# Optimization experiments

Measured on AMD Instinct MI355X. Metric: run time of the kernel, lower is better.

Reference implementation:

```python
import jax, jax.numpy as jnp
import numpy as np

N_RAYS = 32768
N_SAMPLES = N_RAYS * 32  # 1,048,576
FDIM = 32
HID = 64
RGB_HID = 64
THRESHOLD = 1e-4  # early_termination_threshold


def setup_inputs() -> dict:
    key = jax.random.key(0)
    ks = jax.random.split(key, 12)
    # ragged per-ray sample counts (avg 32), adjusted so total is exactly N_SAMPLES
    rng = np.random.default_rng(0)
    counts = rng.integers(8, 57, size=N_RAYS)
    delta = int(N_SAMPLES - counts.sum())
    if delta >= 0:
        counts[:delta] += 1
    else:
        counts[:(-delta)] -= 1
    starts = np.concatenate([[0], np.cumsum(counts)[:-1]])
    packing_info = jnp.asarray(np.stack([starts, counts], axis=1), dtype=jnp.int32)
    ray_ids = jnp.asarray(np.repeat(np.arange(N_RAYS), counts), dtype=jnp.int32)

    pos = jax.random.uniform(ks[0], (N_SAMPLES, 3), minval=-1.0, maxval=1.0)
    dirs = jax.random.normal(ks[1], (N_SAMPLES, 3))
    dirs = dirs / jnp.linalg.norm(dirs, axis=1, keepdims=True)
    dt = jax.random.uniform(ks[2], (N_SAMPLES, 1), minval=0.0, maxval=0.01)
    packed_samples = jnp.concatenate([pos, dirs, dt], axis=1)

    def lin(k, fi, fo):
        return jax.random.normal(k, (fi, fo)) / np.sqrt(fi)

    return {
        "packed_samples": packed_samples,
        "packing_info": packing_info,
        "ray_ids": ray_ids,
        "w1": lin(ks[3], 3, HID), "b1": jnp.zeros(HID),
        "w2": lin(ks[4], HID, FDIM), "b2": jnp.zeros(FDIM),
        "w_sigma": lin(ks[5], FDIM, 1), "b_sigma": jnp.zeros(1),
        "w_rgb1": lin(ks[6], FDIM + 3, RGB_HID), "b_rgb1": jnp.zeros(RGB_HID),
        "w_rgb2": lin(ks[7], RGB_HID, 3), "b_rgb2": jnp.zeros(3),
        "bg_color": jnp.ones(3),
    }


def reference(packed_samples, packing_info, ray_ids, w1, b1, w2, b2,
              w_sigma, b_sigma, w_rgb1, b_rgb1, w_rgb2, b_rgb2, bg_color):
    pos = packed_samples[:, :3]
    dirs = packed_samples[:, 3:6]
    dt = packed_samples[:, 6]

    # feature_module
    feats = jax.nn.relu(pos @ w1 + b1) @ w2 + b2            # [N, FDIM]
    # sigma_decoder
    sigma = jax.nn.softplus(feats @ w_sigma + b_sigma)[:, 0]  # [N]

    # NerfWeights: per-ray transmittance T_i = exp(-sum_{j<i in ray} sigma_j*dt_j),
    # weight_i = T_i * (1 - exp(-sigma_i*dt_i)), zeroed once T drops below threshold.
    tau = sigma * dt
    c_excl = jnp.cumsum(tau) - tau                           # exclusive global cumsum
    seg_base = c_excl[packing_info[:, 0]]                    # cumsum before each ray's start
    T = jnp.exp(-(c_excl - seg_base[ray_ids]))
    alpha = 1.0 - jnp.exp(-tau)
    weights = jnp.where(T > THRESHOLD, T * alpha, 0.0)       # [N]

    # rgb_decoder (masked gather in torch is a perf trick; weight==0 kills masked rgbs)
    h = jax.nn.relu(jnp.concatenate([feats, dirs], axis=1) @ w_rgb1 + b_rgb1)
    rgbs = jax.nn.sigmoid(h @ w_rgb2 + b_rgb2)               # [N, 3]

    contrib = rgbs * weights[:, None]
    rendered = jax.ops.segment_sum(contrib, ray_ids, num_segments=N_RAYS)   # [n_rays,3]
    opac = jax.ops.segment_sum(weights, ray_ids, num_segments=N_RAYS)       # [n_rays]
    return rendered + bg_color * (1.0 - opac[:, None])
```

## Files before the change

kernel.cpp:

```cpp
#include <hip/hip_runtime.h>
#include <hip/hip_bf16.h>
#include <math.h>
#include <stdint.h>

#define N_RAYS    32768
#define N_SAMPLES (N_RAYS * 32)
#define THRESH 0.0001f

typedef __attribute__((ext_vector_type(8))) __bf16 bf16x8;
typedef __attribute__((ext_vector_type(4))) float  f32x4;

union FragU { __hip_bfloat162 h2[4]; uint32_t w[4]; bf16x8 v; };

__device__ inline __hip_bfloat162 pk2(float lo, float hi) {
    float2 t; t.x = lo; t.y = hi;
    return __float22bfloat162_rn(t);
}

__device__ inline bf16x8 pack8(const float* vals) {
    FragU u;
    u.h2[0] = pk2(vals[0], vals[1]);
    u.h2[1] = pk2(vals[2], vals[3]);
    u.h2[2] = pk2(vals[4], vals[5]);
    u.h2[3] = pk2(vals[6], vals[7]);
    return u.v;
}

__device__ inline float rcp_fast(float x) {
    float r;
    asm("v_rcp_f32 %0, %1" : "=v"(r) : "v"(x));
    return r;
}
__device__ inline float sigmoid_fast(float x) { return rcp_fast(1.0f + __expf(-x)); }
__device__ inline float softplus_fast(float x) {
    const float e = __expf(-fabsf(x));
    return fmaxf(x, 0.0f) + __logf(1.0f + e);
}

__global__ __launch_bounds__(256, 2) void nerf_mlp_mfma(
    const float* __restrict__ samples,
    const float* __restrict__ w1,
    const float* __restrict__ b1,
    const float* __restrict__ w2,
    const float* __restrict__ b2,
    const float* __restrict__ w_sigma,
    const float* __restrict__ b_sigma,
    const float* __restrict__ w_rgb1,
    const float* __restrict__ b_rgb1,
    const float* __restrict__ w_rgb2,
    const float* __restrict__ b_rgb2,
    float4* __restrict__ out)
{
    const int lane = threadIdx.x & 63;
    const int g    = lane >> 4;
    const int sl   = lane & 15;

    const int n_waves = (gridDim.x * blockDim.x) >> 6;
    const int wgid    = (blockIdx.x * blockDim.x + threadIdx.x) >> 6;
    const int NPAIR   = N_SAMPLES / 32;

    float cur[2][7] = {{0,0,0,0,0,0,0},{0,0,0,0,0,0,0}};
    if (g == 0 && wgid < NPAIR) {
        const float* s0 = samples + (size_t)(wgid * 32 + sl) * 7;
        const float* s1 = s0 + 16 * 7;
        #pragma unroll
        for (int i = 0; i < 7; ++i) { cur[0][i] = s0[i]; cur[1][i] = s1[i]; }
    }

    bf16x8 A1[4], A2[2][2], Ar1a[4], Ar1b[4], Ar2[2], Ar2f;

    #pragma unroll
    for (int t = 0; t < 4; ++t) {
        float v[8] = {0,0,0,0,0,0,0,0};
        if (g == 0) {
            const int j = t*16 + sl;
            v[0] = w1[j]; v[1] = w1[64+j]; v[2] = w1[128+j]; v[3] = b1[j];
        }
        A1[t] = pack8(v);
    }
    #pragma unroll
    for (int t = 0; t < 2; ++t)
        #pragma unroll
        for (int c = 0; c < 2; ++c) {
            float v[8];
            #pragma unroll
            for (int q = 0; q < 8; ++q) {
                const int j = 16*(2*c + (q>>2)) + 4*g + (q&3);
                v[q] = w2[j*32 + t*16 + sl];
            }
            A2[t][c] = pack8(v);
        }
    #pragma unroll
    for (int t = 0; t < 4; ++t) {
        float v[8];
        #pragma unroll
        for (int q = 0; q < 8; ++q) {
            const int f = 16*(q>>2) + 4*g + (q&3);
            v[q] = w_rgb1[f*64 + t*16 + sl];
        }
        Ar1a[t] = pack8(v);
    }
    #pragma unroll
    for (int t = 0; t < 4; ++t) {
        float v[8] = {0,0,0,0,0,0,0,0};
        if (g == 0) {
            const int j = t*16 + sl;
            v[0] = w_rgb1[32*64 + j]; v[1] = w_rgb1[33*64 + j];
            v[2] = w_rgb1[34*64 + j]; v[3] = b_rgb1[j];
        }
        Ar1b[t] = pack8(v);
    }
    #pragma unroll
    for (int c = 0; c < 2; ++c) {
        float v[8];
        #pragma unroll
        for (int q = 0; q < 8; ++q) {
            const int hh = 16*(2*c + (q>>2)) + 4*g + (q&3);
            v[q] = (sl < 3) ? w_rgb2[hh*3 + sl] : 0.0f;
        }
        Ar2[c] = pack8(v);
    }
    {
        float v[8];
        #pragma unroll
        for (int q = 0; q < 8; ++q) {
            const int f = 16*(q>>2) + 4*g + (q&3);
            v[q] = (sl == 3) ? w_sigma[f] : 0.0f;
        }
        Ar2f = pack8(v);
    }
    f32x4 b2i[2];
    #pragma unroll
    for (int t = 0; t < 2; ++t)
        #pragma unroll
        for (int r = 0; r < 4; ++r)
            b2i[t][r] = b2[16*t + 4*g + r];
    f32x4 arinit;
    arinit[0] = b_rgb2[0]; arinit[1] = b_rgb2[1];
    arinit[2] = b_rgb2[2]; arinit[3] = b_sigma[0];

    const f32x4 zero4 = {0.f, 0.f, 0.f, 0.f};

    for (int pair = wgid; pair < NPAIR; pair += n_waves) {
        float nxt[2][7] = {{0,0,0,0,0,0,0},{0,0,0,0,0,0,0}};
        const int tn = pair + n_waves;
        if (g == 0 && tn < NPAIR) {
            const float* s0 = samples + (size_t)(tn * 32 + sl) * 7;
            const float* s1 = s0 + 16 * 7;
            #pragma unroll
            for (int i = 0; i < 7; ++i) { nxt[0][i] = s0[i]; nxt[1][i] = s1[i]; }
        }

        FragU b1u[2], bd[2];
        #pragma unroll
        for (int s = 0; s < 2; ++s) {
            b1u[s].h2[0] = pk2(cur[s][0], cur[s][1]);
            b1u[s].h2[1] = pk2(cur[s][2], (g==0) ? 1.0f : 0.0f);
            b1u[s].w[2] = 0; b1u[s].w[3] = 0;
            bd[s].h2[0]  = pk2(cur[s][3], cur[s][4]);
            bd[s].h2[1]  = pk2(cur[s][5], (g==0) ? 1.0f : 0.0f);
            bd[s].w[2] = 0; bd[s].w[3] = 0;
        }

        f32x4 accL1[2][4];
        #pragma unroll
        for (int t = 0; t < 4; ++t)
            #pragma unroll
            for (int s = 0; s < 2; ++s)
                accL1[s][t] = __builtin_amdgcn_mfma_f32_16x16x32_bf16(A1[t], b1u[s].v, zero4, 0,0,0);

        FragU B2c[2][2];
        #pragma unroll
        for (int s = 0; s < 2; ++s)
            #pragma unroll
            for (int c = 0; c < 2; ++c) {
                B2c[s][c].h2[0] = pk2(fmaxf(accL1[s][2*c  ][0],0.f), fmaxf(accL1[s][2*c  ][1],0.f));
                B2c[s][c].h2[1] = pk2(fmaxf(accL1[s][2*c  ][2],0.f), fmaxf(accL1[s][2*c  ][3],0.f));
                B2c[s][c].h2[2] = pk2(fmaxf(accL1[s][2*c+1][0],0.f), fmaxf(accL1[s][2*c+1][1],0.f));
                B2c[s][c].h2[3] = pk2(fmaxf(accL1[s][2*c+1][2],0.f), fmaxf(accL1[s][2*c+1][3],0.f));
            }

        f32x4 accL2[2][2];
        #pragma unroll
        for (int t = 0; t < 2; ++t)
            #pragma unroll
            for (int s = 0; s < 2; ++s) {
                accL2[s][t] = __builtin_amdgcn_mfma_f32_16x16x32_bf16(A2[t][0], B2c[s][0].v, b2i[t], 0,0,0);
                accL2[s][t] = __builtin_amdgcn_mfma_f32_16x16x32_bf16(A2[t][1], B2c[s][1].v, accL2[s][t], 0,0,0);
            }
        FragU Bf[2];
        #pragma unroll
        for (int s = 0; s < 2; ++s) {
            Bf[s].h2[0] = pk2(accL2[s][0][0], accL2[s][0][1]);
            Bf[s].h2[1] = pk2(accL2[s][0][2], accL2[s][0][3]);
            Bf[s].h2[2] = pk2(accL2[s][1][0], accL2[s][1][1]);
            Bf[s].h2[3] = pk2(accL2[s][1][2], accL2[s][1][3]);
        }

        f32x4 ah[2][4];
        #pragma unroll
        for (int t = 0; t < 4; ++t)
            #pragma unroll
            for (int s = 0; s < 2; ++s) {
                ah[s][t] = __builtin_amdgcn_mfma_f32_16x16x32_bf16(Ar1a[t], Bf[s].v, zero4, 0,0,0);
                ah[s][t] = __builtin_amdgcn_mfma_f32_16x16x32_bf16(Ar1b[t], bd[s].v, ah[s][t], 0,0,0);
            }
        FragU Bh[2][2];
        #pragma unroll
        for (int s = 0; s < 2; ++s)
            #pragma unroll
            for (int c = 0; c < 2; ++c) {
                Bh[s][c].h2[0] = pk2(fmaxf(ah[s][2*c  ][0],0.f), fmaxf(ah[s][2*c  ][1],0.f));
                Bh[s][c].h2[1] = pk2(fmaxf(ah[s][2*c  ][2],0.f), fmaxf(ah[s][2*c  ][3],0.f));
                Bh[s][c].h2[2] = pk2(fmaxf(ah[s][2*c+1][0],0.f), fmaxf(ah[s][2*c+1][1],0.f));
                Bh[s][c].h2[3] = pk2(fmaxf(ah[s][2*c+1][2],0.f), fmaxf(ah[s][2*c+1][3],0.f));
            }

        f32x4 ar[2];
        #pragma unroll
        for (int s = 0; s < 2; ++s) {
            ar[s] = __builtin_amdgcn_mfma_f32_16x16x32_bf16(Ar2[0], Bh[s][0].v, arinit, 0,0,0);
            ar[s] = __builtin_amdgcn_mfma_f32_16x16x32_bf16(Ar2[1], Bh[s][1].v, ar[s], 0,0,0);
            ar[s] = __builtin_amdgcn_mfma_f32_16x16x32_bf16(Ar2f,   Bf[s].v,    ar[s], 0,0,0);
        }

        #pragma unroll
        for (int s = 0; s < 2; ++s) {
            const float rr    = sigmoid_fast(ar[s][0]);
            const float gg    = sigmoid_fast(ar[s][1]);
            const float bb    = sigmoid_fast(ar[s][2]);
            const float sigma = softplus_fast(ar[s][3]);
            const float tau   = sigma * cur[s][6];
            if (g == 0) out[pair * 32 + s * 16 + sl] = make_float4(tau, rr, gg, bb);
        }

        #pragma unroll
        for (int s = 0; s < 2; ++s)
            #pragma unroll
            for (int i = 0; i < 7; ++i) cur[s][i] = nxt[s][i];
    }
}

__global__ __launch_bounds__(256) void nerf_render_kernel(
    const float4* __restrict__ smp,
    const int*    __restrict__ packing,
    const float*  __restrict__ bg,
    float*        __restrict__ out)
{
    const int gtid = blockIdx.x * blockDim.x + threadIdx.x;
    const int ray  = gtid >> 6;
    const int lane = threadIdx.x & 63;
    if (ray >= N_RAYS) return;

    const int start = packing[2 * ray];
    const int count = packing[2 * ray + 1];

    float tau = 0.0f, r = 0.0f, g = 0.0f, b = 0.0f;
    if (lane < count) {
        const float4 v = smp[start + lane];
        tau = v.x; r = v.y; g = v.z; b = v.w;
    }

    float incl = tau;
    #pragma unroll
    for (int off = 1; off < 64; off <<= 1) {
        const float v = __shfl_up(incl, off, 64);
        if (lane >= off) incl += v;
    }
    const float c_excl = incl - tau;

    const float T     = __expf(-c_excl);
    const float alpha = 1.0f - __expf(-tau);
    float w = (lane < count && T > THRESH) ? T * alpha : 0.0f;

    float cr = r * w, cg = g * w, cb = b * w;

    #pragma unroll
    for (int off = 32; off > 0; off >>= 1) {
        cr += __shfl_down(cr, off, 64);
        cg += __shfl_down(cg, off, 64);
        cb += __shfl_down(cb, off, 64);
        w  += __shfl_down(w,  off, 64);
    }

    if (lane == 0) {
        out[ray * 3 + 0] = cr + bg[0] * (1.0f - w);
        out[ray * 3 + 1] = cg + bg[1] * (1.0f - w);
        out[ray * 3 + 2] = cb + bg[2] * (1.0f - w);
    }
}

extern "C" void kernel_launch(void* const* d_in, const int* in_sizes, int n_in,
                              void* d_out, int out_size, void* d_ws, size_t ws_size,
                              hipStream_t stream) {
    const float* samples  = (const float*)d_in[0];
    const int*   packing  = (const int*)  d_in[1];
    const float* w1       = (const float*)d_in[3];
    const float* b1       = (const float*)d_in[4];
    const float* w2       = (const float*)d_in[5];
    const float* b2       = (const float*)d_in[6];
    const float* w_sigma  = (const float*)d_in[7];
    const float* b_sigma  = (const float*)d_in[8];
    const float* w_rgb1   = (const float*)d_in[9];
    const float* b_rgb1   = (const float*)d_in[10];
    const float* w_rgb2   = (const float*)d_in[11];
    const float* b_rgb2   = (const float*)d_in[12];
    const float* bg       = (const float*)d_in[13];

    float4* smp = (float4*)d_ws;
    float*  out = (float*)d_out;

    nerf_mlp_mfma<<<2048, 256, 0, stream>>>(
        samples, w1, b1, w2, b2, w_sigma, b_sigma,
        w_rgb1, b_rgb1, w_rgb2, b_rgb2, smp);

    nerf_render_kernel<<<(N_RAYS * 64) / 256, 256, 0, stream>>>(smp, packing, bg, out);
}
```

Measured before the change: 54.88 us.

## Use fixed 4-pair tiles per wave with vectorized overlapping sample loads

Replaces the grid-stride loop over 32-sample pairs with a fully unrolled loop over four consecutive pairs per wave (128 samples). Sample rows are loaded with two overlapping 4-wide float loads per row (4-byte aligned) instead of seven scalar loads, and all lanes load rather than only group 0. This cuts load instruction count and loop overhead and lets the next tile's loads be issued ahead of the current tile's compute. It assumes the launch grid exactly covers N_SAMPLES/128 waves, and any launch-config change that this requires is not visible here.

```diff
diff --git a/kernel.cpp b/kernel.cpp
--- a/kernel.cpp
+++ b/kernel.cpp
@@ -9,6 +9,7 @@
 
 typedef __attribute__((ext_vector_type(8))) __bf16 bf16x8;
 typedef __attribute__((ext_vector_type(4))) float  f32x4;
+typedef float f4a __attribute__((ext_vector_type(4), aligned(4)));
 
 union FragU { __hip_bfloat162 h2[4]; uint32_t w[4]; bf16x8 v; };
 
@@ -54,17 +55,15 @@
     const int lane = threadIdx.x & 63;
     const int g    = lane >> 4;
     const int sl   = lane & 15;
-
-    const int n_waves = (gridDim.x * blockDim.x) >> 6;
-    const int wgid    = (blockIdx.x * blockDim.x + threadIdx.x) >> 6;
-    const int NPAIR   = N_SAMPLES / 32;
-
-    float cur[2][7] = {{0,0,0,0,0,0,0},{0,0,0,0,0,0,0}};
-    if (g == 0 && wgid < NPAIR) {
-        const float* s0 = samples + (size_t)(wgid * 32 + sl) * 7;
-        const float* s1 = s0 + 16 * 7;
-        #pragma unroll
-        for (int i = 0; i < 7; ++i) { cur[0][i] = s0[i]; cur[1][i] = s1[i]; }
+    const int wgid = (blockIdx.x * blockDim.x + threadIdx.x) >> 6;
+    const int base0 = wgid * 128;
+
+    f4a sa[4][2], sb[4][2];
+    {
+        const float* sp0 = samples + (size_t)(base0 + sl) * 7;
+        const float* sp1 = samples + (size_t)(base0 + 16 + sl) * 7;
+        sa[0][0] = *(const f4a*)sp0;  sb[0][0] = *(const f4a*)(sp0 + 3);
+        sa[0][1] = *(const f4a*)sp1;  sb[0][1] = *(const f4a*)(sp1 + 3);
     }
 
     bf16x8 A1[4], A2[2][2], Ar1a[4], Ar1b[4], Ar2[2], Ar2f;
@@ -139,26 +138,27 @@
     arinit[0] = b_rgb2[0]; arinit[1] = b_rgb2[1];
     arinit[2] = b_rgb2[2]; arinit[3] = b_sigma[0];
 
+    const float biasone = (g == 0) ? 1.0f : 0.0f;
     const f32x4 zero4 = {0.f, 0.f, 0.f, 0.f};
 
-    for (int pair = wgid; pair < NPAIR; pair += n_waves) {
-        float nxt[2][7] = {{0,0,0,0,0,0,0},{0,0,0,0,0,0,0}};
-        const int tn = pair + n_waves;
-        if (g == 0 && tn < NPAIR) {
-            const float* s0 = samples + (size_t)(tn * 32 + sl) * 7;
-            const float* s1 = s0 + 16 * 7;
-            #pragma unroll
-            for (int i = 0; i < 7; ++i) { nxt[0][i] = s0[i]; nxt[1][i] = s1[i]; }
+    #pragma unroll
+    for (int it = 0; it < 4; ++it) {
+        if (it < 3) {
+            const int nb = base0 + (it + 1) * 32;
+            const float* sp0 = samples + (size_t)(nb + sl) * 7;
+            const float* sp1 = samples + (size_t)(nb + 16 + sl) * 7;
+            sa[it+1][0] = *(const f4a*)sp0;  sb[it+1][0] = *(const f4a*)(sp0 + 3);
+            sa[it+1][1] = *(const f4a*)sp1;  sb[it+1][1] = *(const f4a*)(sp1 + 3);
         }
 
         FragU b1u[2], bd[2];
         #pragma unroll
         for (int s = 0; s < 2; ++s) {
-            b1u[s].h2[0] = pk2(cur[s][0], cur[s][1]);
-            b1u[s].h2[1] = pk2(cur[s][2], (g==0) ? 1.0f : 0.0f);
+            b1u[s].h2[0] = pk2(sa[it][s].x, sa[it][s].y);
+            b1u[s].h2[1] = pk2(sa[it][s].z, biasone);
             b1u[s].w[2] = 0; b1u[s].w[3] = 0;
-            bd[s].h2[0]  = pk2(cur[s][3], cur[s][4]);
-            bd[s].h2[1]  = pk2(cur[s][5], (g==0) ? 1.0f : 0.0f);
+            bd[s].h2[0]  = pk2(sb[it][s].x, sb[it][s].y);
+            bd[s].h2[1]  = pk2(sb[it][s].z, biasone);
             bd[s].w[2] = 0; bd[s].w[3] = 0;
         }
 
@@ -230,14 +230,9 @@
             const float gg    = sigmoid_fast(ar[s][1]);
             const float bb    = sigmoid_fast(ar[s][2]);
             const float sigma = softplus_fast(ar[s][3]);
-            const float tau   = sigma * cur[s][6];
-            if (g == 0) out[pair * 32 + s * 16 + sl] = make_float4(tau, rr, gg, bb);
-        }
-
-        #pragma unroll
-        for (int s = 0; s < 2; ++s)
-            #pragma unroll
-            for (int i = 0; i < 7; ++i) cur[s][i] = nxt[s][i];
+            const float tau   = sigma * sb[it][s].w;
+            if (g == 0) out[base0 + it * 32 + s * 16 + sl] = make_float4(tau, rr, gg, bb);
+        }
     }
 }
 
```

Result: faster. 53.62 us (-2.3%).
